# Kernel tuning notes

Hardware: AMD Instinct MI355X
Metric: run time of the kernel (lower is better)

Reference implementation:

```python
import jax, jax.numpy as jnp
import numpy as np

B, N, K = 1, 1024, 4
E = N * K  # 4096
FV, FE, NH, FOUT = 512, 64, 256, 250


def _sym_norm(a):
    d = a.sum(1)
    di = jnp.where(d > 0, 1.0 / jnp.sqrt(d), 0.0)
    return a * di[:, None] * di[None, :]


def setup_inputs() -> dict:
    key = jax.random.key(0)
    ks = jax.random.split(key, 12)
    # random k-NN style edge pairs (B, N, K, 2)
    ep = jax.random.randint(ks[0], (B, N, K, 2), 0, N)
    s = ep[..., 0].reshape(B, E)
    e = ep[..., 1].reshape(B, E)
    cols = jnp.arange(E)

    def build_T(sb, eb):  # incidence / transition matrix (N, E), duplicates summed
        return jnp.zeros((N, E), jnp.float32).at[sb, cols].add(1.0).at[eb, cols].add(1.0)

    T = jax.vmap(build_T)(s, e)

    def build_adj_e(sb, eb):  # edges adjacent iff they share an endpoint
        m = ((sb[:, None] == sb[None, :]) | (sb[:, None] == eb[None, :]) |
             (eb[:, None] == sb[None, :]) | (eb[:, None] == eb[None, :])).astype(jnp.float32)
        return _sym_norm(m + jnp.eye(E, dtype=jnp.float32))  # plus_one normalize

    adj_e = jax.vmap(build_adj_e)(s, e)

    def build_adj_v(sb, eb):
        a = jnp.zeros((N, N), jnp.float32).at[sb, eb].set(1.0).at[eb, sb].set(1.0)
        return _sym_norm(a)

    adj_v = jax.vmap(build_adj_v)(s, e)

    X = jax.random.normal(ks[1], (B, N, FV), jnp.float32)
    Z = jax.random.normal(ks[2], (B, E, FE), jnp.float32)

    def unif(k, shape, fan_out):  # matches reset_parameters: U(-1/sqrt(out), 1/sqrt(out))
        st = 1.0 / np.sqrt(fan_out)
        return jax.random.uniform(k, shape, jnp.float32, -st, st)

    w1 = unif(ks[3], (FV, NH), NH); b1 = unif(ks[4], (NH,), NH)
    p1 = jax.random.normal(ks[5], (1, FE), jnp.float32)
    w2 = unif(ks[6], (FE, 2 * FE), 2 * FE); b2 = unif(ks[7], (2 * FE,), 2 * FE)
    p2 = jax.random.normal(ks[8], (1, NH), jnp.float32)
    w3 = unif(ks[9], (NH, FOUT), FOUT); b3 = unif(ks[10], (FOUT,), FOUT)
    p3 = jax.random.normal(ks[11], (1, 2 * FE), jnp.float32)
    return dict(X=X, Z=Z, adj_e=adj_e, adj_v=adj_v, T=T,
                w1=w1, p1=p1, b1=b1, w2=w2, p2=p2, b2=b2, w3=w3, p3=p3, b3=b3)


def _node_layer(Hv, He, av, Tb, W, p, bias):
    v = (He @ p.T)[:, 0]                                   # (E,) edge scores
    mult = jnp.einsum('ne,e,me->nm', Tb, v, Tb)            # T diag(v) T^T, (N, N)
    eye = jnp.eye(mult.shape[0], dtype=mult.dtype)
    A = (eye + (1.0 - eye) * mult) * av                    # eye-blend then adj mask
    # NOTE: original computes GELU(output) but then overwrites it with output + bias
    # whenever bias is present (bias=True here), so the activation is discarded.
    return A @ (Hv @ W) + bias


def _edge_layer(Hv, He, ae, Tb, W, p, bias):
    v = (Hv @ p.T)[:, 0]                                   # (N,) node scores
    mult = jnp.einsum('ne,n,nf->ef', Tb, v, Tb)            # T^T diag(v) T, (E, E)
    eye = jnp.eye(mult.shape[0], dtype=mult.dtype)
    A = (eye + (1.0 - eye) * mult) * ae
    A = A / jnp.max(A, axis=0, keepdims=True)              # column-max normalize
    return A @ (He @ W) + bias


def reference(X, Z, adj_e, adj_v, T, w1, p1, b1, w2, p2, b2, w3, p3, b3):
    def single(Hv, He, ae, av, Tb):
        x = jax.nn.relu(_node_layer(Hv, He, av, Tb, w1, p1, b1))  # gc1 (node)
        z = jax.nn.relu(He)
        z = jax.nn.relu(_edge_layer(x, z, ae, Tb, w2, p2, b2))    # gc2 (edge)
        x = _node_layer(x, z, av, Tb, w3, p3, b3)                 # gc3 (node)
        return x, z
    return jax.vmap(single)(X, Z, adj_e, adj_v, T)  # dropout p=0 / eval mode
```

## Files before the change

### kernel.cpp

```cpp
#include <hip/hip_runtime.h>

#define NN 1024
#define NE 4096
#define FVD 512
#define FED 64
#define NHD 256
#define FOUTD 250
#define ICAP 64
#define VCAP 64
#define ECAP 128

__global__ __launch_bounds__(256) void scan_T(
    const float* __restrict__ T, int* __restrict__ se, int* __restrict__ te) {
  size_t i = (size_t)blockIdx.x * blockDim.x + threadIdx.x;
  if (i >= (size_t)NN * NE) return;
  float v = T[i];
  if (v > 0.5f) {
    int n = (int)(i >> 12);
    int e = (int)(i & (NE - 1));
    atomicMin(&se[e], n);
    atomicMax(&te[e], n);
  }
}

__global__ __launch_bounds__(256) void build_inc(
    int* __restrict__ se, int* __restrict__ te,
    int* __restrict__ inc, int* __restrict__ icnt) {
  int e = blockIdx.x * blockDim.x + threadIdx.x;
  if (e >= NE) return;
  int s = se[e], t = te[e];
  if (s < 0 || s >= NN) { s = 0; se[e] = 0; }
  if (t < 0 || t >= NN) { t = s; te[e] = s; }
  int p = atomicAdd(&icnt[s], 1);
  if (p < ICAP) inc[s * ICAP + p] = e;
  if (t != s) {
    p = atomicAdd(&icnt[t], 1);
    if (p < ICAP) inc[t * ICAP + p] = e;
  }
}

__global__ void compact_rows(const float* __restrict__ A, int R, int C, int cap,
                             int* __restrict__ cols, float* __restrict__ vals,
                             float* __restrict__ diag, int* __restrict__ cnt) {
  int wid = (blockIdx.x * blockDim.x + threadIdx.x) >> 6;
  int lane = threadIdx.x & 63;
  if (wid >= R) return;
  const float4* row = (const float4*)(A + (size_t)wid * C);
  int base = 0;
  for (int c0 = 0; c0 < C; c0 += 256) {
    float4 v4 = row[(c0 >> 2) + lane];
    float vv[4] = {v4.x, v4.y, v4.z, v4.w};
    #pragma unroll
    for (int j = 0; j < 4; j++) {
      int c = c0 + lane * 4 + j;
      float v = vv[j];
      if (c == wid) diag[wid] = v;
      bool pred = (v != 0.0f) && (c != wid);
      unsigned long long m = __ballot(pred);
      if (pred) {
        int idx = base + __popcll(m & ((1ull << lane) - 1ull));
        if (idx < cap) {
          cols[(size_t)wid * cap + idx] = c;
          vals[(size_t)wid * cap + idx] = v;
        }
      }
      base += __popcll(m);
    }
  }
  if (lane == 0) cnt[wid] = base < cap ? base : cap;
}

__global__ void wave_dot(const float* __restrict__ X, const float* __restrict__ p,
                         float* __restrict__ out, int rows, int D) {
  int wid = (blockIdx.x * blockDim.x + threadIdx.x) >> 6;
  int lane = threadIdx.x & 63;
  if (wid >= rows) return;
  float acc = 0.0f;
  for (int d = lane; d < D; d += 64) acc += X[(size_t)wid * D + d] * p[d];
  for (int off = 32; off; off >>= 1) acc += __shfl_down(acc, off);
  if (lane == 0) out[wid] = acc;
}

template <bool RELU_A, int N4, int KK, int KSPLIT>
__global__ __launch_bounds__(256) void gemm_f4(
    const float* __restrict__ A, const float* __restrict__ B,
    float* __restrict__ Cpart, int M) {
  constexpr int RPT = 4;
  constexpr int RG = 256 / N4;
  constexpr int KPS = KK / KSPLIT;
  int tid = threadIdx.x;
  int c4 = tid % N4;
  int rg = tid / N4;
  int ks = blockIdx.y;
  int m0 = blockIdx.x * (RG * RPT) + rg * RPT;
  const float4* B4 = (const float4*)B;
  float4 acc[RPT];
  #pragma unroll
  for (int r = 0; r < RPT; r++) acc[r] = make_float4(0.f, 0.f, 0.f, 0.f);
  int kbeg = ks * KPS;
  #pragma unroll 4
  for (int kc = 0; kc < KPS; kc += 4) {
    int k = kbeg + kc;
    float4 b0 = B4[(size_t)(k + 0) * N4 + c4];
    float4 b1 = B4[(size_t)(k + 1) * N4 + c4];
    float4 b2 = B4[(size_t)(k + 2) * N4 + c4];
    float4 b3 = B4[(size_t)(k + 3) * N4 + c4];
    #pragma unroll
    for (int r = 0; r < RPT; r++) {
      float4 a = *(const float4*)(A + (size_t)(m0 + r) * KK + k);
      if (RELU_A) {
        a.x = fmaxf(a.x, 0.f); a.y = fmaxf(a.y, 0.f);
        a.z = fmaxf(a.z, 0.f); a.w = fmaxf(a.w, 0.f);
      }
      acc[r].x += a.x * b0.x; acc[r].y += a.x * b0.y; acc[r].z += a.x * b0.z; acc[r].w += a.x * b0.w;
      acc[r].x += a.y * b1.x; acc[r].y += a.y * b1.y; acc[r].z += a.y * b1.z; acc[r].w += a.y * b1.w;
      acc[r].x += a.z * b2.x; acc[r].y += a.z * b2.y; acc[r].z += a.z * b2.z; acc[r].w += a.z * b2.w;
      acc[r].x += a.w * b3.x; acc[r].y += a.w * b3.y; acc[r].z += a.w * b3.z; acc[r].w += a.w * b3.w;
    }
  }
  float4* out = (float4*)Cpart + ((size_t)ks * M + m0) * N4 + c4;
  #pragma unroll
  for (int r = 0; r < RPT; r++) out[(size_t)r * N4] = acc[r];
}

__global__ void reduce_part(const float4* __restrict__ part, float4* __restrict__ out,
                            int n4, int ksplit) {
  int i = blockIdx.x * blockDim.x + threadIdx.x;
  int stride = gridDim.x * blockDim.x;
  for (; i < n4; i += stride) {
    float4 s = part[i];
    for (int k = 1; k < ksplit; k++) {
      float4 p = part[(size_t)k * n4 + i];
      s.x += p.x; s.y += p.y; s.z += p.z; s.w += p.w;
    }
    out[i] = s;
  }
}

__global__ void pad_w3(const float* __restrict__ w3, float* __restrict__ w3p) {
  int i = blockIdx.x * blockDim.x + threadIdx.x;
  if (i >= 256 * 256) return;
  int r = i >> 8, c = i & 255;
  w3p[i] = (c < FOUTD) ? w3[r * FOUTD + c] : 0.f;
}

template <bool RELU>
__global__ __launch_bounds__(256) void node_apply(
    const float* __restrict__ HW, int H, int ldH, const float* __restrict__ v,
    const int* __restrict__ se, const int* __restrict__ te,
    const int* __restrict__ inc, const int* __restrict__ icnt,
    const int* __restrict__ avc, const float* __restrict__ avv,
    const float* __restrict__ avd, const int* __restrict__ avcnt,
    const float* __restrict__ bias, float* __restrict__ out) {
  int n = blockIdx.x;
  __shared__ float scoef[VCAP];
  __shared__ int scol[VCAP];
  int cnt = avcnt[n];
  int tid = threadIdx.x;
  if (tid < cnt) {
    int m = avc[n * VCAP + tid];
    float mult = 0.0f;
    int ic = icnt[n]; if (ic > ICAP) ic = ICAP;
    for (int k = 0; k < ic; k++) {
      int e = inc[n * ICAP + k];
      int s = se[e], t = te[e];
      float wn = (float)((s == n) + (t == n));
      float wm = (float)((s == m) + (t == m));
      mult += wn * v[e] * wm;
    }
    scoef[tid] = mult * avv[n * VCAP + tid];
    scol[tid] = m;
  }
  __syncthreads();
  float d = avd[n];
  for (int h = tid; h < H; h += 256) {
    float acc = d * HW[(size_t)n * ldH + h];
    for (int k = 0; k < cnt; k++)
      acc += scoef[k] * HW[(size_t)scol[k] * ldH + h];
    acc += bias[h];
    if (RELU) acc = fmaxf(acc, 0.0f);
    out[(size_t)n * H + h] = acc;
  }
}

__global__ __launch_bounds__(256) void edge_coef(
    const float* __restrict__ v2, const int* __restrict__ se, const int* __restrict__ te,
    const int* __restrict__ aec, const float* __restrict__ aev,
    const float* __restrict__ aed, const int* __restrict__ aecnt,
    float* __restrict__ coef, float* __restrict__ rmax) {
  int i = blockIdx.x * blockDim.x + threadIdx.x;
  if (i >= NE) return;
  int s = se[i], t = te[i];
  float vs = v2[s], vt = v2[t];
  int cnt = aecnt[i];
  float mx = aed[i];
  for (int k = 0; k < cnt; k++) {
    int j = aec[i * ECAP + k];
    int sj = se[j], tj = te[j];
    float m;
    if (s == t) {
      m = 2.0f * vs * (float)((sj == s) + (tj == s));
    } else {
      m = vs * (float)((sj == s) + (tj == s)) + vt * (float)((sj == t) + (tj == t));
    }
    float c = m * aev[i * ECAP + k];
    coef[i * ECAP + k] = c;
    mx = fmaxf(mx, c);
  }
  rmax[i] = mx;
}

__global__ __launch_bounds__(128) void edge_apply(
    const float* __restrict__ ZW, const int* __restrict__ aec,
    const float* __restrict__ coef, const float* __restrict__ aed,
    const int* __restrict__ aecnt, const float* __restrict__ rmax,
    const float* __restrict__ bias, float* __restrict__ out) {
  int i = blockIdx.x;
  int h = threadIdx.x;
  __shared__ float sw[ECAP];
  __shared__ int sj[ECAP];
  int cnt = aecnt[i];
  if (h < cnt) {
    int j = aec[i * ECAP + h];
    sj[h] = j;
    sw[h] = coef[i * ECAP + h] / rmax[j];
  }
  __syncthreads();
  float acc = (aed[i] / rmax[i]) * ZW[(size_t)i * 128 + h];
  for (int k = 0; k < cnt; k++)
    acc += sw[k] * ZW[(size_t)sj[k] * 128 + h];
  acc += bias[h];
  out[(size_t)i * 128 + h] = fmaxf(acc, 0.0f);
}

extern "C" void kernel_launch(void* const* d_in, const int* in_sizes, int n_in,
                              void* d_out, int out_size, void* d_ws, size_t ws_size,
                              hipStream_t stream) {
  const float* X    = (const float*)d_in[0];
  const float* Z    = (const float*)d_in[1];
  const float* adjE = (const float*)d_in[2];
  const float* adjV = (const float*)d_in[3];
  const float* T    = (const float*)d_in[4];
  const float* w1   = (const float*)d_in[5];
  const float* p1   = (const float*)d_in[6];
  const float* b1   = (const float*)d_in[7];
  const float* w2   = (const float*)d_in[8];
  const float* p2   = (const float*)d_in[9];
  const float* b2   = (const float*)d_in[10];
  const float* w3   = (const float*)d_in[11];
  const float* p3   = (const float*)d_in[12];
  const float* b3   = (const float*)d_in[13];

  float* xout = (float*)d_out;
  float* zout = xout + (size_t)NN * FOUTD;

  char* w = (char*)d_ws;
  auto alloc = [&](size_t bytes) {
    char* p = w;
    w += (bytes + 255) & ~(size_t)255;
    return p;
  };
  int*   se    = (int*)alloc(NE * 4);
  int*   te    = (int*)alloc(NE * 4);
  int*   icnt  = (int*)alloc(NN * 4);
  int*   inc   = (int*)alloc((size_t)NN * ICAP * 4);
  int*   avc   = (int*)alloc((size_t)NN * VCAP * 4);
  float* avv   = (float*)alloc((size_t)NN * VCAP * 4);
  float* avd   = (float*)alloc(NN * 4);
  int*   avcnt = (int*)alloc(NN * 4);
  int*   aec   = (int*)alloc((size_t)NE * ECAP * 4);
  float* aev   = (float*)alloc((size_t)NE * ECAP * 4);
  float* aed   = (float*)alloc(NE * 4);
  int*   aecnt = (int*)alloc(NE * 4);
  float* coef2 = (float*)alloc((size_t)NE * ECAP * 4);
  float* rmax  = (float*)alloc(NE * 4);
  float* v1    = (float*)alloc(NE * 4);
  float* v2    = (float*)alloc(NN * 4);
  float* v3    = (float*)alloc(NE * 4);
  float* HW1   = (float*)alloc((size_t)NN * NHD * 4);
  float* x1    = (float*)alloc((size_t)NN * NHD * 4);
  float* ZW2   = (float*)alloc((size_t)NE * 128 * 4);
  float* XW3p  = (float*)alloc((size_t)NN * 256 * 4);
  float* w3p   = (float*)alloc(256 * 256 * 4);
  float* gpart = (float*)alloc((size_t)8 * NN * NHD * 4);
  (void)ws_size; (void)in_sizes; (void)n_in; (void)out_size;

  hipMemsetAsync(icnt, 0, NN * 4, stream);
  hipMemsetAsync(se, 0x7f, NE * 4, stream);
  hipMemsetAsync(te, 0xff, NE * 4, stream);

  scan_T<<<(NN * NE) / 256, 256, 0, stream>>>(T, se, te);
  build_inc<<<NE / 256, 256, 0, stream>>>(se, te, inc, icnt);
  compact_rows<<<NN * 64 / 256, 256, 0, stream>>>(adjV, NN, NN, VCAP, avc, avv, avd, avcnt);
  compact_rows<<<NE * 64 / 256, 256, 0, stream>>>(adjE, NE, NE, ECAP, aec, aev, aed, aecnt);
  pad_w3<<<256, 256, 0, stream>>>(w3, w3p);

  wave_dot<<<NE * 64 / 256, 256, 0, stream>>>(Z, p1, v1, NE, FED);
  gemm_f4<false, 64, 512, 8><<<dim3(64, 8), 256, 0, stream>>>(X, w1, gpart, NN);
  reduce_part<<<512, 256, 0, stream>>>((const float4*)gpart, (float4*)HW1,
                                       NN * NHD / 4, 8);
  node_apply<true><<<NN, 256, 0, stream>>>(HW1, NHD, NHD, v1, se, te, inc, icnt,
                                           avc, avv, avd, avcnt, b1, x1);

  wave_dot<<<NN * 64 / 256, 256, 0, stream>>>(x1, p2, v2, NN, NHD);
  gemm_f4<true, 32, 64, 4><<<dim3(128, 4), 256, 0, stream>>>(Z, w2, gpart, NE);
  reduce_part<<<512, 256, 0, stream>>>((const float4*)gpart, (float4*)ZW2,
                                       NE * 128 / 4, 4);
  edge_coef<<<NE / 256, 256, 0, stream>>>(v2, se, te, aec, aev, aed, aecnt, coef2, rmax);
  edge_apply<<<NE, 128, 0, stream>>>(ZW2, aec, coef2, aed, aecnt, rmax, b2, zout);

  wave_dot<<<NE * 64 / 256, 256, 0, stream>>>(zout, p3, v3, NE, 128);
  gemm_f4<false, 64, 256, 8><<<dim3(64, 8), 256, 0, stream>>>(x1, w3p, gpart, NN);
  reduce_part<<<512, 256, 0, stream>>>((const float4*)gpart, (float4*)XW3p,
                                       NN * 256 / 4, 8);
  node_apply<false><<<NN, 256, 0, stream>>>(XW3p, FOUTD, 256, v3, se, te, inc, icnt,
                                            avc, avv, avd, avcnt, b3, xout);
}
```

Measured before the change: 266.4 us.

## Fuse init, compaction, dot products and split-K reductions to cut kernel launches

Merges the memsets, w3 padding, first node-score dot and output zeroing into a single init kernel, and runs both adjacency compactions in one launch. The split-K GEMMs now accumulate directly into their outputs with atomicAdd, which removes the partial buffer and the reduce kernels. The score dot products p2 and p3 move into the epilogues of node_apply and edge_apply as block reductions. The goal is fewer launches and less memory traffic, at the cost of atomic contention and summation order that is no longer deterministic.

```diff
diff --git a/kernel.cpp b/kernel.cpp
--- a/kernel.cpp
+++ b/kernel.cpp
@@ -9,6 +9,32 @@
 #define ICAP 64
 #define VCAP 64
 #define ECAP 128
+
+__global__ __launch_bounds__(256) void init_fused(
+    const float* __restrict__ Z, const float* __restrict__ p1,
+    const float* __restrict__ w3,
+    int* __restrict__ se, int* __restrict__ te, int* __restrict__ icnt,
+    float* __restrict__ w3p, float4* __restrict__ HW1z,
+    float4* __restrict__ ZW2z, float4* __restrict__ XW3pz,
+    float* __restrict__ v1) {
+  int gtid = blockIdx.x * 256 + threadIdx.x;
+  int wid = gtid >> 6, lane = gtid & 63;
+  if (wid < NE) {
+    float val = Z[(size_t)wid * FED + lane] * p1[lane];
+    for (int off = 32; off; off >>= 1) val += __shfl_down(val, off);
+    if (lane == 0) v1[wid] = val;
+  }
+  if (gtid < NE) { se[gtid] = 0x7fffffff; te[gtid] = -1; }
+  if (gtid < NN) icnt[gtid] = 0;
+  if (gtid < 256 * 256) {
+    int r = gtid >> 8, c = gtid & 255;
+    w3p[gtid] = (c < FOUTD) ? w3[r * FOUTD + c] : 0.f;
+  }
+  const float4 z4 = make_float4(0.f, 0.f, 0.f, 0.f);
+  if (gtid < 65536)  HW1z[gtid] = z4;
+  if (gtid < 131072) ZW2z[gtid] = z4;
+  if (gtid < 65536)  XW3pz[gtid] = z4;
+}
 
 __global__ __launch_bounds__(256) void scan_T(
     const float* __restrict__ T, int* __restrict__ se, int* __restrict__ te) {
@@ -39,12 +65,10 @@
   }
 }
 
-__global__ void compact_rows(const float* __restrict__ A, int R, int C, int cap,
-                             int* __restrict__ cols, float* __restrict__ vals,
-                             float* __restrict__ diag, int* __restrict__ cnt) {
-  int wid = (blockIdx.x * blockDim.x + threadIdx.x) >> 6;
-  int lane = threadIdx.x & 63;
-  if (wid >= R) return;
+__device__ __forceinline__ void compact_row(
+    const float* __restrict__ A, int wid, int lane, int C, int cap,
+    int* __restrict__ cols, float* __restrict__ vals,
+    float* __restrict__ diag, int* __restrict__ cnt) {
   const float4* row = (const float4*)(A + (size_t)wid * C);
   int base = 0;
   for (int c0 = 0; c0 < C; c0 += 256) {
@@ -70,21 +94,25 @@
   if (lane == 0) cnt[wid] = base < cap ? base : cap;
 }
 
-__global__ void wave_dot(const float* __restrict__ X, const float* __restrict__ p,
-                         float* __restrict__ out, int rows, int D) {
-  int wid = (blockIdx.x * blockDim.x + threadIdx.x) >> 6;
+__global__ void compact_both(
+    const float* __restrict__ adjV, const float* __restrict__ adjE,
+    int* __restrict__ avc, float* __restrict__ avv, float* __restrict__ avd,
+    int* __restrict__ avcnt,
+    int* __restrict__ aec, float* __restrict__ aev, float* __restrict__ aed,
+    int* __restrict__ aecnt) {
+  int gw = (blockIdx.x * blockDim.x + threadIdx.x) >> 6;
   int lane = threadIdx.x & 63;
-  if (wid >= rows) return;
-  float acc = 0.0f;
-  for (int d = lane; d < D; d += 64) acc += X[(size_t)wid * D + d] * p[d];
-  for (int off = 32; off; off >>= 1) acc += __shfl_down(acc, off);
-  if (lane == 0) out[wid] = acc;
+  if (gw < NN) {
+    compact_row(adjV, gw, lane, NN, VCAP, avc, avv, avd, avcnt);
+  } else if (gw < NN + NE) {
+    compact_row(adjE, gw - NN, lane, NE, ECAP, aec, aev, aed, aecnt);
+  }
 }
 
 template <bool RELU_A, int N4, int KK, int KSPLIT>
-__global__ __launch_bounds__(256) void gemm_f4(
+__global__ __launch_bounds__(256) void gemm_f4_atomic(
     const float* __restrict__ A, const float* __restrict__ B,
-    float* __restrict__ Cpart, int M) {
+    float* __restrict__ C, int M) {
   constexpr int RPT = 4;
   constexpr int RG = 256 / N4;
   constexpr int KPS = KK / KSPLIT;
@@ -118,43 +146,29 @@
       acc[r].x += a.w * b3.x; acc[r].y += a.w * b3.y; acc[r].z += a.w * b3.z; acc[r].w += a.w * b3.w;
     }
   }
-  float4* out = (float4*)Cpart + ((size_t)ks * M + m0) * N4 + c4;
   #pragma unroll
-  for (int r = 0; r < RPT; r++) out[(size_t)r * N4] = acc[r];
-}
-
-__global__ void reduce_part(const float4* __restrict__ part, float4* __restrict__ out,
-                            int n4, int ksplit) {
-  int i = blockIdx.x * blockDim.x + threadIdx.x;
-  int stride = gridDim.x * blockDim.x;
-  for (; i < n4; i += stride) {
-    float4 s = part[i];
-    for (int k = 1; k < ksplit; k++) {
-      float4 p = part[(size_t)k * n4 + i];
-      s.x += p.x; s.y += p.y; s.z += p.z; s.w += p.w;
-    }
-    out[i] = s;
-  }
-}
-
-__global__ void pad_w3(const float* __restrict__ w3, float* __restrict__ w3p) {
-  int i = blockIdx.x * blockDim.x + threadIdx.x;
-  if (i >= 256 * 256) return;
-  int r = i >> 8, c = i & 255;
-  w3p[i] = (c < FOUTD) ? w3[r * FOUTD + c] : 0.f;
-}
-
-template <bool RELU>
+  for (int r = 0; r < RPT; r++) {
+    float* o = C + ((size_t)(m0 + r) * N4 + c4) * 4;
+    atomicAdd(o + 0, acc[r].x);
+    atomicAdd(o + 1, acc[r].y);
+    atomicAdd(o + 2, acc[r].z);
+    atomicAdd(o + 3, acc[r].w);
+  }
+}
+
+template <bool RELU, bool FUSE>
 __global__ __launch_bounds__(256) void node_apply(
     const float* __restrict__ HW, int H, int ldH, const float* __restrict__ v,
     const int* __restrict__ se, const int* __restrict__ te,
     const int* __restrict__ inc, const int* __restrict__ icnt,
     const int* __restrict__ avc, const float* __restrict__ avv,
     const float* __restrict__ avd, const int* __restrict__ avcnt,
-    const float* __restrict__ bias, float* __restrict__ out) {
+    const float* __restrict__ bias, float* __restrict__ out,
+    const float* __restrict__ pvec, float* __restrict__ vout) {
   int n = blockIdx.x;
   __shared__ float scoef[VCAP];
   __shared__ int scol[VCAP];
+  __shared__ float red[256];
   int cnt = avcnt[n];
   int tid = threadIdx.x;
   if (tid < cnt) {
@@ -173,6 +187,7 @@
   }
   __syncthreads();
   float d = avd[n];
+  float part = 0.0f;
   for (int h = tid; h < H; h += 256) {
     float acc = d * HW[(size_t)n * ldH + h];
     for (int k = 0; k < cnt; k++)
@@ -180,6 +195,16 @@
     acc += bias[h];
     if (RELU) acc = fmaxf(acc, 0.0f);
     out[(size_t)n * H + h] = acc;
+    if (FUSE) part += acc * pvec[h];
+  }
+  if (FUSE) {
+    red[tid] = part;
+    __syncthreads();
+    for (int s = 128; s; s >>= 1) {
+      if (tid < s) red[tid] += red[tid + s];
+      __syncthreads();
+    }
+    if (tid == 0) vout[n] = red[0];
   }
 }
 
@@ -214,11 +239,13 @@
     const float* __restrict__ ZW, const int* __restrict__ aec,
     const float* __restrict__ coef, const float* __restrict__ aed,
     const int* __restrict__ aecnt, const float* __restrict__ rmax,
-    const float* __restrict__ bias, float* __restrict__ out) {
+    const float* __restrict__ bias, float* __restrict__ out,
+    const float* __restrict__ p3, float* __restrict__ v3) {
   int i = blockIdx.x;
   int h = threadIdx.x;
   __shared__ float sw[ECAP];
   __shared__ int sj[ECAP];
+  __shared__ float red[128];
   int cnt = aecnt[i];
   if (h < cnt) {
     int j = aec[i * ECAP + h];
@@ -230,7 +257,15 @@
   for (int k = 0; k < cnt; k++)
     acc += sw[k] * ZW[(size_t)sj[k] * 128 + h];
   acc += bias[h];
-  out[(size_t)i * 128 + h] = fmaxf(acc, 0.0f);
+  acc = fmaxf(acc, 0.0f);
+  out[(size_t)i * 128 + h] = acc;
+  red[h] = acc * p3[h];
+  __syncthreads();
+  for (int s = 64; s; s >>= 1) {
+    if (h < s) red[h] += red[h + s];
+    __syncthreads();
+  }
+  if (h == 0) v3[i] = red[0];
 }
 
 extern "C" void kernel_launch(void* const* d_in, const int* in_sizes, int n_in,
@@ -282,37 +317,25 @@
   float* ZW2   = (float*)alloc((size_t)NE * 128 * 4);
   float* XW3p  = (float*)alloc((size_t)NN * 256 * 4);
   float* w3p   = (float*)alloc(256 * 256 * 4);
-  float* gpart = (float*)alloc((size_t)8 * NN * NHD * 4);
   (void)ws_size; (void)in_sizes; (void)n_in; (void)out_size;
 
-  hipMemsetAsync(icnt, 0, NN * 4, stream);
-  hipMemsetAsync(se, 0x7f, NE * 4, stream);
-  hipMemsetAsync(te, 0xff, NE * 4, stream);
-
+  init_fused<<<1024, 256, 0, stream>>>(Z, p1, w3, se, te, icnt, w3p,
+                                       (float4*)HW1, (float4*)ZW2, (float4*)XW3p, v1);
   scan_T<<<(NN * NE) / 256, 256, 0, stream>>>(T, se, te);
   build_inc<<<NE / 256, 256, 0, stream>>>(se, te, inc, icnt);
-  compact_rows<<<NN * 64 / 256, 256, 0, stream>>>(adjV, NN, NN, VCAP, avc, avv, avd, avcnt);
-  compact_rows<<<NE * 64 / 256, 256, 0, stream>>>(adjE, NE, NE, ECAP, aec, aev, aed, aecnt);
-  pad_w3<<<256, 256, 0, stream>>>(w3, w3p);
-
-  wave_dot<<<NE * 64 / 256, 256, 0, stream>>>(Z, p1, v1, NE, FED);
-  gemm_f4<false, 64, 512, 8><<<dim3(64, 8), 256, 0, stream>>>(X, w1, gpart, NN);
-  reduce_part<<<512, 256, 0, stream>>>((const float4*)gpart, (float4*)HW1,
-                                       NN * NHD / 4, 8);
-  node_apply<true><<<NN, 256, 0, stream>>>(HW1, NHD, NHD, v1, se, te, inc, icnt,
-                                           avc, avv, avd, avcnt, b1, x1);
-
-  wave_dot<<<NN * 64 / 256, 256, 0, stream>>>(x1, p2, v2, NN, NHD);
-  gemm_f4<true, 32, 64, 4><<<dim3(128, 4), 256, 0, stream>>>(Z, w2, gpart, NE);
-  reduce_part<<<512, 256, 0, stream>>>((const float4*)gpart, (float4*)ZW2,
-                                       NE * 128 / 4, 4);
+  compact_both<<<(NN + NE) * 64 / 256, 256, 0, stream>>>(
+      adjV, adjE, avc, avv, avd, avcnt, aec, aev, aed, aecnt);
+
+  gemm_f4_atomic<false, 64, 512, 8><<<dim3(64, 8), 256, 0, stream>>>(X, w1, HW1, NN);
+  node_apply<true, true><<<NN, 256, 0, stream>>>(HW1, NHD, NHD, v1, se, te, inc, icnt,
+                                                 avc, avv, avd, avcnt, b1, x1, p2, v2);
+
+  gemm_f4_atomic<true, 32, 64, 4><<<dim3(128, 4), 256, 0, stream>>>(Z, w2, ZW2, NE);
   edge_coef<<<NE / 256, 256, 0, stream>>>(v2, se, te, aec, aev, aed, aecnt, coef2, rmax);
-  edge_apply<<<NE, 128, 0, stream>>>(ZW2, aec, coef2, aed, aecnt, rmax, b2, zout);
-
-  wave_dot<<<NE * 64 / 256, 256, 0, stream>>>(zout, p3, v3, NE, 128);
-  gemm_f4<false, 64, 256, 8><<<dim3(64, 8), 256, 0, stream>>>(x1, w3p, gpart, NN);
-  reduce_part<<<512, 256, 0, stream>>>((const float4*)gpart, (float4*)XW3p,
-                                       NN * 256 / 4, 8);
-  node_apply<false><<<NN, 256, 0, stream>>>(XW3p, FOUTD, 256, v3, se, te, inc, icnt,
-                                            avc, avv, avd, avcnt, b3, xout);
-}
+  edge_apply<<<NE, 128, 0, stream>>>(ZW2, aec, coef2, aed, aecnt, rmax, b2, zout, p3, v3);
+
+  gemm_f4_atomic<false, 64, 256, 8><<<dim3(64, 8), 256, 0, stream>>>(x1, w3p, XW3p, NN);
+  node_apply<false, false><<<NN, 256, 0, stream>>>(XW3p, FOUTD, 256, v3, se, te, inc, icnt,
+                                                   avc, avv, avd, avcnt, b3, xout,
+                                                   nullptr, nullptr);
+}
```

New measurement: 307.5 us. 1.15x slower.
